# Kernel optimization log

Measured on AMD Instinct MI355X. Metric: run time of the kernel, lower is better.

## Reference

```python
import jax, jax.numpy as jnp
import numpy as np

E = 1024
H = 16
D = E // H
T = 1024
S = 1024
B = 8
MASK_FILL = 1e-30  # note: module fills masked scores with 1e-30, NOT -inf


def setup_inputs() -> dict:
    key = jax.random.key(0)
    ks = jax.random.split(key, 8)
    inp = {
        "query1": jax.random.normal(ks[0], (T, B, E), jnp.float32),
        "query2": jax.random.normal(ks[1], (T, B, E), jnp.float32),
        "key": jax.random.normal(ks[2], (S, B, E), jnp.float32),
        "value": jax.random.normal(ks[3], (S, B, E), jnp.float32),
        # causal mask: True = masked
        "attn_mask": jnp.triu(jnp.ones((T, S), jnp.bool_), k=1),
        # xavier-uniform-ish weights (torch stores Linear weight as [out, in])
        "q_w": jax.random.uniform(ks[4], (E, E), jnp.float32, -1, 1) * np.sqrt(6.0 / (2 * E)),
        "k_w": jax.random.uniform(ks[5], (E, E), jnp.float32, -1, 1) * np.sqrt(6.0 / (2 * E)),
        "v_w": jax.random.uniform(ks[6], (E, E), jnp.float32, -1, 1) * np.sqrt(6.0 / (2 * E)),
        "out_w": jax.random.uniform(ks[7], (E, E), jnp.float32, -1, 1) * np.sqrt(6.0 / (2 * E)),
    }
    return inp


def _split_heads(x):
    # [L, B, E] -> [B, H, L, D]
    L = x.shape[0]
    return x.reshape(L, B, H, D).transpose(1, 2, 0, 3)


def reference(query1, query2, key, value, attn_mask, q_w, k_w, v_w, out_w):
    scaling = float(D) ** -0.5
    q1 = _split_heads(query1 @ q_w.T) * scaling  # [B,H,T,D]
    q2 = _split_heads(query2 @ q_w.T) * scaling
    k = _split_heads(key @ k_w.T)                # [B,H,S,D]
    v = _split_heads(value @ v_w.T)

    # ---- stream s (second query stream attends first) ----
    scores_s = jnp.einsum("bhtd,bhsd->bhts", q2, k)
    scores_s = jnp.where(attn_mask[None, None], MASK_FILL, scores_s)
    probs_s = jax.nn.softmax(scores_s, axis=-1)
    o_s = jnp.einsum("bhts,bhsd->bhtd", probs_s, v)  # [B,H,T,D]

    # k/v update between passes (requires T == S)
    k2 = k + o_s
    v2 = v + o_s

    # ---- stream d ----
    scores_d = jnp.einsum("bhtd,bhsd->bhts", q1, k2)
    scores_d = jnp.where(attn_mask[None, None], MASK_FILL, scores_d)
    probs_d = jax.nn.softmax(scores_d, axis=-1)
    o_d = jnp.einsum("bhts,bhsd->bhtd", probs_d, v2)

    def _merge_and_proj(o):
        # [B,H,T,D] -> [T,B,E] -> out proj (no bias)
        return o.transpose(2, 0, 1, 3).reshape(T, B, E) @ out_w.T

    attn_output_s = _merge_and_proj(o_s)
    attn_output_d = _merge_and_proj(o_d)
    attn_s = probs_s.mean(axis=1)  # [B,T,S]
    attn_d = probs_d.mean(axis=1)
    return attn_output_d, attn_d, attn_output_s, attn_s
```

## Files before the change

### kernel.cpp

```cpp
#include <hip/hip_runtime.h>
#include <cstddef>

#define T_DIM 1024
#define S_DIM 1024
#define B_DIM 8
#define E_DIM 1024
#define H_DIM 16
#define D_DIM 64
#define NBHTD (B_DIM*H_DIM*T_DIM*D_DIM)

typedef __attribute__((ext_vector_type(8))) short short8;
typedef __attribute__((ext_vector_type(4))) short short4v;
typedef __attribute__((ext_vector_type(4))) float floatx4;

__device__ inline unsigned short f2bf(float x){
    union { float f; unsigned u; } v; v.f = x;
    unsigned r = (v.u + 0x7FFFu + ((v.u >> 16) & 1u)) >> 16;
    return (unsigned short)r;
}
__device__ inline float bf2f(unsigned short h){
    union { float f; unsigned u; } v; v.u = ((unsigned)h) << 16; return v.f;
}

typedef __attribute__((address_space(1))) const unsigned int* gptr_t;
typedef __attribute__((address_space(3))) unsigned int* lptr_t;
__device__ inline void gl_lds16(const void* g, void* l){
    __builtin_amdgcn_global_load_lds((gptr_t)g, (lptr_t)l, 16, 0, 0);
}

__device__ inline int poff(int row, int s){
    return (row << 10) + ((((s >> 3) ^ (row & 7)) << 3)) + (s & 7);
}

__global__ __launch_bounds__(256)
void split_pair(const float* __restrict__ src, unsigned short* __restrict__ hi,
                unsigned short* __restrict__ lo, float scale)
{
    size_t i = ((size_t)blockIdx.x*256 + threadIdx.x)*8;
    float4 a = *(const float4*)(src+i);
    float4 b = *(const float4*)(src+i+4);
    float v[8] = {a.x,a.y,a.z,a.w,b.x,b.y,b.z,b.w};
    short8 h8, l8;
    #pragma unroll
    for (int j = 0; j < 8; ++j) {
        float x = v[j]*scale;
        unsigned short hh = f2bf(x);
        h8[j] = (short)hh;
        l8[j] = (short)f2bf(x - bf2f(hh));
    }
    *(short8*)(hi+i) = h8;
    *(short8*)(lo+i) = l8;
}

template <int AMODE, int CMODE>
__global__ __launch_bounds__(256, 2)
void gemm_bf3(const unsigned short* __restrict__ Ahi, const unsigned short* __restrict__ Alo,
              const unsigned short* __restrict__ Bhi, const unsigned short* __restrict__ Blo,
              float* __restrict__ Cf,
              unsigned short* __restrict__ Chi, unsigned short* __restrict__ Clo)
{
    __shared__ __align__(16) unsigned short lds[4][128*32];

    const int tid  = threadIdx.x;
    const int n0   = blockIdx.x * 128;
    const int m0   = blockIdx.y * 128;
    const int wave = tid >> 6, lane = tid & 63;
    const int lrow = lane & 15, quad = lane >> 4;
    const int mw = (wave & 1)*64, nw = (wave >> 1)*64;

    floatx4 acc[4][4];
    #pragma unroll
    for (int i = 0; i < 4; ++i)
        #pragma unroll
        for (int j = 0; j < 4; ++j) acc[i][j] = (floatx4){0.f,0.f,0.f,0.f};

    for (int kk = 0; kk < 1024; kk += 32) {
        __syncthreads();
        #pragma unroll
        for (int rnd = 0; rnd < 2; ++rnd) {
            int c = rnd*256 + tid;
            int row = c >> 2, col8 = (c & 3)*8;
            size_t aoff;
            if (AMODE == 0) {
                aoff = (size_t)(m0+row)*1024 + kk + col8;
            } else {
                int r = m0 + row; int t = r >> 3, bb = r & 7;
                int h = kk >> 6, d0 = (kk & 63) + col8;
                aoff = (((size_t)(bb*H_DIM + h)*T_DIM) + t)*D_DIM + d0;
            }
            size_t boff = (size_t)(n0+row)*1024 + kk + col8;
            gl_lds16(Ahi + aoff, &lds[0][c*8]);
            gl_lds16(Alo + aoff, &lds[1][c*8]);
            gl_lds16(Bhi + boff, &lds[2][c*8]);
            gl_lds16(Blo + boff, &lds[3][c*8]);
        }
        __syncthreads();

        short8 ah[4], al[4], bh[4], bl[4];
        #pragma unroll
        for (int mt = 0; mt < 4; ++mt) {
            int r = mw + mt*16 + lrow;
            ah[mt] = *(const short8*)&lds[0][r*32 + quad*8];
            al[mt] = *(const short8*)&lds[1][r*32 + quad*8];
        }
        #pragma unroll
        for (int nt = 0; nt < 4; ++nt) {
            int r = nw + nt*16 + lrow;
            bh[nt] = *(const short8*)&lds[2][r*32 + quad*8];
            bl[nt] = *(const short8*)&lds[3][r*32 + quad*8];
        }
        #pragma unroll
        for (int mt = 0; mt < 4; ++mt)
            #pragma unroll
            for (int nt = 0; nt < 4; ++nt) {
                acc[mt][nt] = __builtin_amdgcn_mfma_f32_16x16x32_bf16(ah[mt], bh[nt], acc[mt][nt], 0,0,0);
                acc[mt][nt] = __builtin_amdgcn_mfma_f32_16x16x32_bf16(ah[mt], bl[nt], acc[mt][nt], 0,0,0);
                acc[mt][nt] = __builtin_amdgcn_mfma_f32_16x16x32_bf16(al[mt], bh[nt], acc[mt][nt], 0,0,0);
            }
    }

    #pragma unroll
    for (int mt = 0; mt < 4; ++mt) {
        #pragma unroll
        for (int nt = 0; nt < 4; ++nt) {
            int n = n0 + nw + nt*16 + lrow;
            #pragma unroll
            for (int r = 0; r < 4; ++r) {
                int m = m0 + mw + mt*16 + quad*4 + r;
                float v = acc[mt][nt][r];
                if (CMODE == 2) {
                    Cf[(size_t)m*1024 + n] = v;
                } else {
                    int t = m >> 3, bb = m & 7;
                    int h = n >> 6, d = n & 63;
                    size_t idx = (((size_t)(bb*H_DIM + h)*T_DIM) + t)*D_DIM + d;
                    if (CMODE == 0) {
                        Cf[idx] = v;
                    } else {
                        unsigned short hh = f2bf(v);
                        Chi[idx] = hh;
                        Clo[idx] = f2bf(v - bf2f(hh));
                    }
                }
            }
        }
    }
}

__global__ __launch_bounds__(256)
void split_vt(const float* __restrict__ Vh, unsigned short* __restrict__ Vthi,
              unsigned short* __restrict__ Vtlo)
{
    __shared__ float tile[64][68];
    const int bh = blockIdx.y, s0 = blockIdx.x*64;
    const int tid = threadIdx.x;
    const size_t base = (size_t)bh*S_DIM*D_DIM;

    {
        int r = tid >> 2, c0 = (tid & 3) * 16;
        const float* p = Vh + base + (size_t)(s0 + r)*D_DIM + c0;
        float4 a = *(const float4*)p;
        float4 b = *(const float4*)(p+4);
        float4 c = *(const float4*)(p+8);
        float4 d = *(const float4*)(p+12);
        *(float4*)&tile[r][c0]    = a;
        *(float4*)&tile[r][c0+4]  = b;
        *(float4*)&tile[r][c0+8]  = c;
        *(float4*)&tile[r][c0+12] = d;
    }
    __syncthreads();
    {
        int d = tid >> 2, cs = (tid & 3) * 16;
        short8 hi[2], lo[2];
        #pragma unroll
        for (int half = 0; half < 2; ++half)
            #pragma unroll
            for (int u = 0; u < 8; ++u) {
                float x = tile[cs + half*8 + u][d];
                unsigned short hh = f2bf(x);
                hi[half][u] = (short)hh;
                lo[half][u] = (short)f2bf(x - bf2f(hh));
            }
        size_t obase = base + (size_t)d*S_DIM + s0 + cs;
        *(short8*)(Vthi + obase)     = hi[0];
        *(short8*)(Vthi + obase + 8) = hi[1];
        *(short8*)(Vtlo + obase)     = lo[0];
        *(short8*)(Vtlo + obase + 8) = lo[1];
    }
}

__global__ __launch_bounds__(256, 2)
void attn_mfma(const float* __restrict__ Qh,
               const unsigned short* __restrict__ Khi, const unsigned short* __restrict__ Klo,
               const unsigned short* __restrict__ Vthi, const unsigned short* __restrict__ Vtlo,
               float* __restrict__ Ofp,
               unsigned short* __restrict__ Ohi, unsigned short* __restrict__ Olo,
               float* __restrict__ attn_mean)
{
    const int bid = blockIdx.x;
    const int b   = bid & 7;
    const int t0  = (bid >> 3) * 16;
    const int tid  = threadIdx.x;
    const int lane = tid & 63;
    const int wave = tid >> 6;
    const int lrow = lane & 15;
    const int quad = lane >> 4;
    const int t_g  = t0 + lrow;

    __shared__ __align__(16) unsigned short plds[16*1024];
    __shared__ float2 stats[4][16];

    float accm[64];
    #pragma unroll
    for (int i = 0; i < 64; ++i) accm[i] = 0.f;

    #pragma unroll 1
    for (int h = 0; h < H_DIM; ++h) {
        const int bh = b*H_DIM + h;
        const size_t kbase = (size_t)bh * S_DIM * D_DIM;

        short8 qh0, ql0, qh1, ql1;
        {
            const float* qp = Qh + kbase + (size_t)(t0 + lrow)*D_DIM + quad*8;
            float4 a  = *(const float4*)qp;
            float4 b4 = *(const float4*)(qp+4);
            float4 c4 = *(const float4*)(qp+32);
            float4 d4 = *(const float4*)(qp+36);
            float va[8]  = {a.x,a.y,a.z,a.w,b4.x,b4.y,b4.z,b4.w};
            float vb8[8] = {c4.x,c4.y,c4.z,c4.w,d4.x,d4.y,d4.z,d4.w};
            #pragma unroll
            for (int j = 0; j < 8; ++j) {
                unsigned short h0 = f2bf(va[j]);
                qh0[j] = (short)h0; ql0[j] = (short)f2bf(va[j] - bf2f(h0));
                unsigned short h1 = f2bf(vb8[j]);
                qh1[j] = (short)h1; ql1[j] = (short)f2bf(vb8[j] - bf2f(h1));
            }
        }

        float sv[64];
        {
            const unsigned short* kph = Khi + kbase + (size_t)(wave*256 + lrow)*D_DIM + quad*8;
            const unsigned short* kpl = Klo + kbase + (size_t)(wave*256 + lrow)*D_DIM + quad*8;
            short8 kh0 = *(const short8*)(kph);
            short8 kh1 = *(const short8*)(kph + 32);
            short8 kl0 = *(const short8*)(kpl);
            short8 kl1 = *(const short8*)(kpl + 32);
            #pragma unroll
            for (int jt = 0; jt < 16; ++jt) {
                short8 nh0, nh1, nl0, nl1;
                if (jt < 15) {
                    const unsigned short* nph = kph + (jt+1)*16*D_DIM;
                    const unsigned short* npl = kpl + (jt+1)*16*D_DIM;
                    nh0 = *(const short8*)(nph);
                    nh1 = *(const short8*)(nph + 32);
                    nl0 = *(const short8*)(npl);
                    nl1 = *(const short8*)(npl + 32);
                }
                floatx4 acc = {0.f,0.f,0.f,0.f};
                acc = __builtin_amdgcn_mfma_f32_16x16x32_bf16(kh0, qh0, acc, 0,0,0);
                acc = __builtin_amdgcn_mfma_f32_16x16x32_bf16(kh1, qh1, acc, 0,0,0);
                acc = __builtin_amdgcn_mfma_f32_16x16x32_bf16(kl0, qh0, acc, 0,0,0);
                acc = __builtin_amdgcn_mfma_f32_16x16x32_bf16(kl1, qh1, acc, 0,0,0);
                acc = __builtin_amdgcn_mfma_f32_16x16x32_bf16(kh0, ql0, acc, 0,0,0);
                acc = __builtin_amdgcn_mfma_f32_16x16x32_bf16(kh1, ql1, acc, 0,0,0);
                const int sb = wave*256 + jt*16 + quad*4;
                #pragma unroll
                for (int r = 0; r < 4; ++r)
                    sv[jt*4+r] = (sb + r > t_g) ? 1e-30f : acc[r];
                kh0 = nh0; kh1 = nh1; kl0 = nl0; kl1 = nl1;
            }
        }

        float mt[32];
        #pragma unroll
        for (int i = 0; i < 32; ++i) mt[i] = fmaxf(sv[i], sv[i+32]);
        #pragma unroll
        for (int st = 16; st > 0; st >>= 1) {
            #pragma unroll
            for (int i = 0; i < st; ++i) mt[i] = fmaxf(mt[i], mt[i+st]);
        }
        float m_loc = fmaxf(mt[0], __shfl_xor(mt[0], 16));
        m_loc = fmaxf(m_loc, __shfl_xor(m_loc, 32));

        #pragma unroll
        for (int i = 0; i < 64; ++i) sv[i] = __expf(sv[i] - m_loc);
        float st2[32];
        #pragma unroll
        for (int i = 0; i < 32; ++i) st2[i] = sv[i] + sv[i+32];
        #pragma unroll
        for (int st = 16; st > 0; st >>= 1) {
            #pragma unroll
            for (int i = 0; i < st; ++i) st2[i] += st2[i+st];
        }
        float s_loc = st2[0] + __shfl_xor(st2[0], 16);
        s_loc += __shfl_xor(s_loc, 32);

        if (quad == 0) stats[wave][lrow] = make_float2(m_loc, s_loc);
        __syncthreads();

        float2 c0 = stats[0][lrow], c1 = stats[1][lrow];
        float2 c2 = stats[2][lrow], c3 = stats[3][lrow];
        float m_g = fmaxf(fmaxf(c0.x, c1.x), fmaxf(c2.x, c3.x));
        float sum_g = c0.y*__expf(c0.x - m_g) + c1.y*__expf(c1.x - m_g)
                    + c2.y*__expf(c2.x - m_g) + c3.y*__expf(c3.x - m_g);
        const float myscale = __expf(m_loc - m_g) / sum_g;

        #pragma unroll
        for (int jt = 0; jt < 16; ++jt) {
            float p0 = sv[jt*4+0]*myscale, p1 = sv[jt*4+1]*myscale;
            float p2 = sv[jt*4+2]*myscale, p3 = sv[jt*4+3]*myscale;
            accm[jt*4+0] += p0; accm[jt*4+1] += p1;
            accm[jt*4+2] += p2; accm[jt*4+3] += p3;
            short4v pk;
            pk[0] = (short)f2bf(p0); pk[1] = (short)f2bf(p1);
            pk[2] = (short)f2bf(p2); pk[3] = (short)f2bf(p3);
            const int sidx = wave*256 + jt*16 + quad*4;
            *(short4v*)&plds[poff(lrow, sidx)] = pk;
        }
        __syncthreads();

        {
            const int d0 = wave*16;
            const unsigned short* vh = Vthi + kbase + (size_t)(d0 + lrow)*S_DIM;
            const unsigned short* vl = Vtlo + kbase + (size_t)(d0 + lrow)*S_DIM;
            floatx4 oa = {0.f,0.f,0.f,0.f}, ob = {0.f,0.f,0.f,0.f};
            #pragma unroll 4
            for (int sk = 0; sk < S_DIM; sk += 32) {
                const int sa = sk + quad*8;
                short8 af  = *(const short8*)&plds[poff(lrow, sa)];
                short8 bh8 = *(const short8*)(vh + sa);
                short8 bl8 = *(const short8*)(vl + sa);
                oa = __builtin_amdgcn_mfma_f32_16x16x32_bf16(af, bh8, oa, 0,0,0);
                ob = __builtin_amdgcn_mfma_f32_16x16x32_bf16(af, bl8, ob, 0,0,0);
            }
            #pragma unroll
            for (int r = 0; r < 4; ++r) {
                int q = quad*4 + r;
                float v = oa[r] + ob[r];
                size_t idx = kbase + (size_t)(t0+q)*D_DIM + d0 + lrow;
                if (Ofp) Ofp[idx] = v;
                unsigned short hh = f2bf(v);
                Ohi[idx] = hh;
                Olo[idx] = f2bf(v - bf2f(hh));
            }
        }
    }

    {
        float* am = attn_mean + ((size_t)b*T_DIM + t_g)*S_DIM + wave*256 + quad*4;
        #pragma unroll
        for (int jt = 0; jt < 16; ++jt) {
            float4 p4;
            p4.x = accm[jt*4+0]*(1.0f/H_DIM);
            p4.y = accm[jt*4+1]*(1.0f/H_DIM);
            p4.z = accm[jt*4+2]*(1.0f/H_DIM);
            p4.w = accm[jt*4+3]*(1.0f/H_DIM);
            *(float4*)(am + jt*16) = p4;
        }
    }
}

__global__ __launch_bounds__(256)
void add_k(unsigned short* __restrict__ Khi, unsigned short* __restrict__ Klo,
           const float* __restrict__ O)
{
    size_t i = ((size_t)blockIdx.x*256 + threadIdx.x)*8;
    short8 hi = *(short8*)(Khi+i), lo = *(short8*)(Klo+i);
    float4 o0 = *(const float4*)(O+i), o1 = *(const float4*)(O+i+4);
    float ov[8] = {o0.x,o0.y,o0.z,o0.w,o1.x,o1.y,o1.z,o1.w};
    short8 nh, nl;
    #pragma unroll
    for (int j = 0; j < 8; ++j) {
        float k = bf2f((unsigned short)hi[j]) + bf2f((unsigned short)lo[j]) + ov[j];
        unsigned short hh = f2bf(k);
        nh[j] = (short)hh;
        nl[j] = (short)f2bf(k - bf2f(hh));
    }
    *(short8*)(Khi+i) = nh;
    *(short8*)(Klo+i) = nl;
}

__global__ __launch_bounds__(256)
void add_v(float* __restrict__ V, const float* __restrict__ O)
{
    size_t i = ((size_t)blockIdx.x*256 + threadIdx.x)*4;
    float4 o = *(const float4*)(O+i);
    float4 v = *(const float4*)(V+i);
    v.x+=o.x; v.y+=o.y; v.z+=o.z; v.w+=o.w;
    *(float4*)(V+i) = v;
}

extern "C" void kernel_launch(void* const* d_in, const int* in_sizes, int n_in,
                              void* d_out, int out_size, void* d_ws, size_t ws_size,
                              hipStream_t stream)
{
    const float* q1  = (const float*)d_in[0];
    const float* q2  = (const float*)d_in[1];
    const float* key = (const float*)d_in[2];
    const float* val = (const float*)d_in[3];
    const float* qw  = (const float*)d_in[5];
    const float* kw  = (const float*)d_in[6];
    const float* vw  = (const float*)d_in[7];
    const float* ow  = (const float*)d_in[8];

    float* out   = (float*)d_out;
    float* outd  = out;
    float* attnd = out + 1*(size_t)NBHTD;
    float* outs  = out + 2*(size_t)NBHTD;
    float* attns = out + 3*(size_t)NBHTD;

    unsigned short* ws_u16 = (unsigned short*)d_ws;
    unsigned short* Khi  = ws_u16;
    unsigned short* Klo  = Khi  + (size_t)NBHTD;
    unsigned short* Vthi = Klo  + (size_t)NBHTD;
    unsigned short* Vtlo = Vthi + (size_t)NBHTD;
    unsigned short* R2a  = Vtlo + (size_t)NBHTD;
    unsigned short* R2b  = R2a  + 2*(size_t)NBHTD;

    const size_t EE = (size_t)E_DIM*E_DIM;
    unsigned short* qwhi = R2a;
    unsigned short* qwlo = qwhi + EE;
    unsigned short* kwhi = qwlo + EE;
    unsigned short* kwlo = kwhi + EE;
    unsigned short* vwhi = kwlo + EE;
    unsigned short* vwlo = vwhi + EE;
    float* Osb = (float*)R2a;
    unsigned short* Odhi = R2a;
    unsigned short* Odlo = Odhi + (size_t)NBHTD;
    unsigned short* Oshi = R2b;
    unsigned short* Oslo = Oshi + (size_t)NBHTD;
    unsigned short* owhi = ws_u16;
    unsigned short* owlo = owhi + EE;

    float* Q1h = outd;
    float* Q2h = outs;
    float* Vh  = attnd;
    unsigned short* Ahi = (unsigned short*)attns;
    unsigned short* Alo = Ahi + (size_t)NBHTD;

    const dim3 ggrid(8, 64);

    split_pair<<<512, 256, 0, stream>>>(qw, qwhi, qwlo, 1.f);
    split_pair<<<512, 256, 0, stream>>>(kw, kwhi, kwlo, 1.f);
    split_pair<<<512, 256, 0, stream>>>(vw, vwhi, vwlo, 1.f);

    split_pair<<<4096, 256, 0, stream>>>(key, Ahi, Alo, 1.f);
    gemm_bf3<0,1><<<ggrid, 256, 0, stream>>>(Ahi, Alo, kwhi, kwlo, nullptr, Khi, Klo);

    split_pair<<<4096, 256, 0, stream>>>(val, Ahi, Alo, 1.f);
    gemm_bf3<0,0><<<ggrid, 256, 0, stream>>>(Ahi, Alo, vwhi, vwlo, Vh, nullptr, nullptr);
    split_vt<<<dim3(16, 128), 256, 0, stream>>>(Vh, Vthi, Vtlo);

    split_pair<<<4096, 256, 0, stream>>>(q1, Ahi, Alo, 0.125f);
    gemm_bf3<0,0><<<ggrid, 256, 0, stream>>>(Ahi, Alo, qwhi, qwlo, Q1h, nullptr, nullptr);

    split_pair<<<4096, 256, 0, stream>>>(q2, Ahi, Alo, 0.125f);
    gemm_bf3<0,0><<<ggrid, 256, 0, stream>>>(Ahi, Alo, qwhi, qwlo, Q2h, nullptr, nullptr);

    attn_mfma<<<dim3(512), 256, 0, stream>>>(Q2h, Khi, Klo, Vthi, Vtlo,
                                             Osb, Oshi, Oslo, attns);

    add_k<<<4096, 256, 0, stream>>>(Khi, Klo, Osb);
    add_v<<<8192, 256, 0, stream>>>(Vh, Osb);
    split_vt<<<dim3(16, 128), 256, 0, stream>>>(Vh, Vthi, Vtlo);

    attn_mfma<<<dim3(512), 256, 0, stream>>>(Q1h, Khi, Klo, Vthi, Vtlo,
                                             nullptr, Odhi, Odlo, attnd);

    split_pair<<<512, 256, 0, stream>>>(ow, owhi, owlo, 1.f);
    gemm_bf3<1,2><<<ggrid, 256, 0, stream>>>(Oshi, Oslo, owhi, owlo, outs, nullptr, nullptr);
    gemm_bf3<1,2><<<ggrid, 256, 0, stream>>>(Odhi, Odlo, owhi, owlo, outd, nullptr, nullptr);
}
```

Measured before the change: 1.625 ms.

## Double attention block to 8 waves, splitting S range and reducing PV via LDS

The attention kernel now launches 512 threads (8 waves) per block instead of 256. Each wave handles 128 keys instead of 256, which halves the per-thread score, probability and attn-mean register arrays. The P·V stage splits the S dimension in two halves across wave groups, and the partial outputs are combined through a new shared buffer behind an extra barrier. This aims to cut register pressure and raise the number of waves resident per CU to hide latency, at the cost of an extra sync and LDS reduction per head.

```diff
diff --git a/kernel.cpp b/kernel.cpp
--- a/kernel.cpp
+++ b/kernel.cpp
@@ -189,7 +189,7 @@
     }
 }
 
-__global__ __launch_bounds__(256, 2)
+__global__ __launch_bounds__(512, 2)
 void attn_mfma(const float* __restrict__ Qh,
                const unsigned short* __restrict__ Khi, const unsigned short* __restrict__ Klo,
                const unsigned short* __restrict__ Vthi, const unsigned short* __restrict__ Vtlo,
@@ -208,11 +208,12 @@
     const int t_g  = t0 + lrow;
 
     __shared__ __align__(16) unsigned short plds[16*1024];
-    __shared__ float2 stats[4][16];
-
-    float accm[64];
+    __shared__ float2 stats[8][16];
+    __shared__ float  pbuf[4][16][16];
+
+    float accm[32];
     #pragma unroll
-    for (int i = 0; i < 64; ++i) accm[i] = 0.f;
+    for (int i = 0; i < 32; ++i) accm[i] = 0.f;
 
     #pragma unroll 1
     for (int h = 0; h < H_DIM; ++h) {
@@ -237,18 +238,18 @@
             }
         }
 
-        float sv[64];
+        float sv[32];
         {
-            const unsigned short* kph = Khi + kbase + (size_t)(wave*256 + lrow)*D_DIM + quad*8;
-            const unsigned short* kpl = Klo + kbase + (size_t)(wave*256 + lrow)*D_DIM + quad*8;
+            const unsigned short* kph = Khi + kbase + (size_t)(wave*128 + lrow)*D_DIM + quad*8;
+            const unsigned short* kpl = Klo + kbase + (size_t)(wave*128 + lrow)*D_DIM + quad*8;
             short8 kh0 = *(const short8*)(kph);
             short8 kh1 = *(const short8*)(kph + 32);
             short8 kl0 = *(const short8*)(kpl);
             short8 kl1 = *(const short8*)(kpl + 32);
             #pragma unroll
-            for (int jt = 0; jt < 16; ++jt) {
+            for (int jt = 0; jt < 8; ++jt) {
                 short8 nh0, nh1, nl0, nl1;
-                if (jt < 15) {
+                if (jt < 7) {
                     const unsigned short* nph = kph + (jt+1)*16*D_DIM;
                     const unsigned short* npl = kpl + (jt+1)*16*D_DIM;
                     nh0 = *(const short8*)(nph);
@@ -263,7 +264,7 @@
                 acc = __builtin_amdgcn_mfma_f32_16x16x32_bf16(kl1, qh1, acc, 0,0,0);
                 acc = __builtin_amdgcn_mfma_f32_16x16x32_bf16(kh0, ql0, acc, 0,0,0);
                 acc = __builtin_amdgcn_mfma_f32_16x16x32_bf16(kh1, ql1, acc, 0,0,0);
-                const int sb = wave*256 + jt*16 + quad*4;
+                const int sb = wave*128 + jt*16 + quad*4;
                 #pragma unroll
                 for (int r = 0; r < 4; ++r)
                     sv[jt*4+r] = (sb + r > t_g) ? 1e-30f : acc[r];
@@ -271,11 +272,11 @@
             }
         }
 
-        float mt[32];
-        #pragma unroll
-        for (int i = 0; i < 32; ++i) mt[i] = fmaxf(sv[i], sv[i+32]);
-        #pragma unroll
-        for (int st = 16; st > 0; st >>= 1) {
+        float mt[16];
+        #pragma unroll
+        for (int i = 0; i < 16; ++i) mt[i] = fmaxf(sv[i], sv[i+16]);
+        #pragma unroll
+        for (int st = 8; st > 0; st >>= 1) {
             #pragma unroll
             for (int i = 0; i < st; ++i) mt[i] = fmaxf(mt[i], mt[i+st]);
         }
@@ -283,12 +284,12 @@
         m_loc = fmaxf(m_loc, __shfl_xor(m_loc, 32));
 
         #pragma unroll
-        for (int i = 0; i < 64; ++i) sv[i] = __expf(sv[i] - m_loc);
-        float st2[32];
-        #pragma unroll
-        for (int i = 0; i < 32; ++i) st2[i] = sv[i] + sv[i+32];
-        #pragma unroll
-        for (int st = 16; st > 0; st >>= 1) {
+        for (int i = 0; i < 32; ++i) sv[i] = __expf(sv[i] - m_loc);
+        float st2[16];
+        #pragma unroll
+        for (int i = 0; i < 16; ++i) st2[i] = sv[i] + sv[i+16];
+        #pragma unroll
+        for (int st = 8; st > 0; st >>= 1) {
             #pragma unroll
             for (int i = 0; i < st; ++i) st2[i] += st2[i+st];
         }
@@ -298,15 +299,23 @@
         if (quad == 0) stats[wave][lrow] = make_float2(m_loc, s_loc);
         __syncthreads();
 
-        float2 c0 = stats[0][lrow], c1 = stats[1][lrow];
-        float2 c2 = stats[2][lrow], c3 = stats[3][lrow];
-        float m_g = fmaxf(fmaxf(c0.x, c1.x), fmaxf(c2.x, c3.x));
-        float sum_g = c0.y*__expf(c0.x - m_g) + c1.y*__expf(c1.x - m_g)
-                    + c2.y*__expf(c2.x - m_g) + c3.y*__expf(c3.x - m_g);
+        float m_g, sum_g;
+        {
+            float2 c0 = stats[0][lrow], c1 = stats[1][lrow];
+            float2 c2 = stats[2][lrow], c3 = stats[3][lrow];
+            float2 c4 = stats[4][lrow], c5 = stats[5][lrow];
+            float2 c6 = stats[6][lrow], c7 = stats[7][lrow];
+            m_g = fmaxf(fmaxf(fmaxf(c0.x, c1.x), fmaxf(c2.x, c3.x)),
+                        fmaxf(fmaxf(c4.x, c5.x), fmaxf(c6.x, c7.x)));
+            sum_g = c0.y*__expf(c0.x - m_g) + c1.y*__expf(c1.x - m_g)
+                  + c2.y*__expf(c2.x - m_g) + c3.y*__expf(c3.x - m_g)
+                  + c4.y*__expf(c4.x - m_g) + c5.y*__expf(c5.x - m_g)
+                  + c6.y*__expf(c6.x - m_g) + c7.y*__expf(c7.x - m_g);
+        }
         const float myscale = __expf(m_loc - m_g) / sum_g;
 
         #pragma unroll
-        for (int jt = 0; jt < 16; ++jt) {
+        for (int jt = 0; jt < 8; ++jt) {
             float p0 = sv[jt*4+0]*myscale, p1 = sv[jt*4+1]*myscale;
             float p2 = sv[jt*4+2]*myscale, p3 = sv[jt*4+3]*myscale;
             accm[jt*4+0] += p0; accm[jt*4+1] += p1;
@@ -314,42 +323,51 @@
             short4v pk;
             pk[0] = (short)f2bf(p0); pk[1] = (short)f2bf(p1);
             pk[2] = (short)f2bf(p2); pk[3] = (short)f2bf(p3);
-            const int sidx = wave*256 + jt*16 + quad*4;
+            const int sidx = wave*128 + jt*16 + quad*4;
             *(short4v*)&plds[poff(lrow, sidx)] = pk;
         }
         __syncthreads();
 
         {
-            const int d0 = wave*16;
+            const int d0    = (wave & 3)*16;
+            const int shalf = (wave >> 2)*512;
             const unsigned short* vh = Vthi + kbase + (size_t)(d0 + lrow)*S_DIM;
             const unsigned short* vl = Vtlo + kbase + (size_t)(d0 + lrow)*S_DIM;
             floatx4 oa = {0.f,0.f,0.f,0.f}, ob = {0.f,0.f,0.f,0.f};
             #pragma unroll 4
-            for (int sk = 0; sk < S_DIM; sk += 32) {
-                const int sa = sk + quad*8;
+            for (int sk = 0; sk < 512; sk += 32) {
+                const int sa = shalf + sk + quad*8;
                 short8 af  = *(const short8*)&plds[poff(lrow, sa)];
                 short8 bh8 = *(const short8*)(vh + sa);
                 short8 bl8 = *(const short8*)(vl + sa);
                 oa = __builtin_amdgcn_mfma_f32_16x16x32_bf16(af, bh8, oa, 0,0,0);
                 ob = __builtin_amdgcn_mfma_f32_16x16x32_bf16(af, bl8, ob, 0,0,0);
             }
-            #pragma unroll
-            for (int r = 0; r < 4; ++r) {
-                int q = quad*4 + r;
-                float v = oa[r] + ob[r];
-                size_t idx = kbase + (size_t)(t0+q)*D_DIM + d0 + lrow;
-                if (Ofp) Ofp[idx] = v;
-                unsigned short hh = f2bf(v);
-                Ohi[idx] = hh;
-                Olo[idx] = f2bf(v - bf2f(hh));
+            if (wave >= 4) {
+                #pragma unroll
+                for (int r = 0; r < 4; ++r)
+                    pbuf[wave-4][quad*4+r][lrow] = oa[r] + ob[r];
+            }
+            __syncthreads();
+            if (wave < 4) {
+                #pragma unroll
+                for (int r = 0; r < 4; ++r) {
+                    int q = quad*4 + r;
+                    float v = oa[r] + ob[r] + pbuf[wave][q][lrow];
+                    size_t idx = kbase + (size_t)(t0+q)*D_DIM + d0 + lrow;
+                    if (Ofp) Ofp[idx] = v;
+                    unsigned short hh = f2bf(v);
+                    Ohi[idx] = hh;
+                    Olo[idx] = f2bf(v - bf2f(hh));
+                }
             }
         }
     }
 
     {
-        float* am = attn_mean + ((size_t)b*T_DIM + t_g)*S_DIM + wave*256 + quad*4;
-        #pragma unroll
-        for (int jt = 0; jt < 16; ++jt) {
+        float* am = attn_mean + ((size_t)b*T_DIM + t_g)*S_DIM + wave*128 + quad*4;
+        #pragma unroll
+        for (int jt = 0; jt < 8; ++jt) {
             float4 p4;
             p4.x = accm[jt*4+0]*(1.0f/H_DIM);
             p4.y = accm[jt*4+1]*(1.0f/H_DIM);
@@ -457,14 +475,14 @@
     split_pair<<<4096, 256, 0, stream>>>(q2, Ahi, Alo, 0.125f);
     gemm_bf3<0,0><<<ggrid, 256, 0, stream>>>(Ahi, Alo, qwhi, qwlo, Q2h, nullptr, nullptr);
 
-    attn_mfma<<<dim3(512), 256, 0, stream>>>(Q2h, Khi, Klo, Vthi, Vtlo,
+    attn_mfma<<<dim3(512), 512, 0, stream>>>(Q2h, Khi, Klo, Vthi, Vtlo,
                                              Osb, Oshi, Oslo, attns);
 
     add_k<<<4096, 256, 0, stream>>>(Khi, Klo, Osb);
     add_v<<<8192, 256, 0, stream>>>(Vh, Osb);
     split_vt<<<dim3(16, 128), 256, 0, stream>>>(Vh, Vthi, Vtlo);
 
-    attn_mfma<<<dim3(512), 256, 0, stream>>>(Q1h, Khi, Klo, Vthi, Vtlo,
+    attn_mfma<<<dim3(512), 512, 0, stream>>>(Q1h, Khi, Klo, Vthi, Vtlo,
                                              nullptr, Odhi, Odlo, attnd);
 
     split_pair<<<512, 256, 0, stream>>>(ow, owhi, owlo, 1.f);
```

New measurement: 1.724 ms. +6.1%, slower.
